# Kernel optimization log

Measured on AMD Instinct MI355X. Metric: run time of the kernel, lower is better.

The kernel has to match this reference:

```python
import jax, jax.numpy as jnp
import numpy as np

B, L, D_MODEL = 4, 2048, 1024
D_STATE, D_CONV, EXPAND, HEADDIM = 128, 4, 2, 64
D_INNER = EXPAND * D_MODEL            # 2048
NHEADS = D_INNER // HEADDIM           # 32
CONV_DIM = D_INNER + 2 * D_STATE      # 2304
D_IN_PROJ = 2 * D_INNER + 2 * D_STATE + NHEADS  # 4448
EPS = 1e-5


def _silu(v):
    return v * jax.nn.sigmoid(v)


def setup_inputs() -> dict:
    key = jax.random.key(0)
    ks = jax.random.split(key, 8)
    x = jax.random.normal(ks[0], (B, L, D_MODEL), dtype=jnp.float32)
    ln_w = jnp.ones((D_MODEL,), jnp.float32)
    ln_b = jnp.zeros((D_MODEL,), jnp.float32)
    in_proj_w = jax.random.normal(ks[1], (D_IN_PROJ, D_MODEL), jnp.float32) * 0.02
    conv_w = jax.random.normal(ks[2], (CONV_DIM, D_CONV), jnp.float32) * 0.2
    conv_b = jnp.zeros((CONV_DIM,), jnp.float32)
    # inverse-softplus of dt sampled in [1e-3, 1e-1], matching mamba2 dt init
    dt_bias = jnp.log(jnp.expm1(jax.random.uniform(ks[3], (NHEADS,), minval=0.001, maxval=0.1)))
    # A sampled uniform in [1,16], stored as log (A = -exp(A_log))
    A_log = jnp.log(jax.random.uniform(ks[4], (NHEADS,), minval=1.0, maxval=16.0))
    D = jnp.ones((NHEADS,), jnp.float32)
    rms_w = jnp.ones((D_INNER,), jnp.float32)
    out_proj_w = jax.random.normal(ks[5], (D_MODEL, D_INNER), jnp.float32) * 0.02
    return {"x": x, "ln_w": ln_w, "ln_b": ln_b, "in_proj_w": in_proj_w,
            "conv_w": conv_w, "conv_b": conv_b, "dt_bias": dt_bias,
            "A_log": A_log, "D": D, "rms_w": rms_w, "out_proj_w": out_proj_w}


def reference(x, ln_w, ln_b, in_proj_w, conv_w, conv_b, dt_bias, A_log, D, rms_w, out_proj_w):
    b = x.shape[0]
    # LayerNorm
    mu = x.mean(-1, keepdims=True)
    var = ((x - mu) ** 2).mean(-1, keepdims=True)
    u = (x - mu) * jax.lax.rsqrt(var + EPS) * ln_w + ln_b
    # input projection -> z | xBC | dt
    zxbcdt = jnp.einsum('bld,ed->ble', u, in_proj_w)
    z = zxbcdt[..., :D_INNER]
    xBC = zxbcdt[..., D_INNER:D_INNER + CONV_DIM]
    dt = jax.nn.softplus(zxbcdt[..., -NHEADS:] + dt_bias)  # (b,l,h)
    # causal depthwise conv along time (kernel D_CONV) + silu
    xpad = jnp.pad(xBC, ((0, 0), (D_CONV - 1, 0), (0, 0)))
    conv = conv_b + sum(conv_w[:, k] * xpad[:, k:k + L, :] for k in range(D_CONV))
    xBC = _silu(conv)
    xh = xBC[..., :D_INNER].reshape(b, L, NHEADS, HEADDIM)       # (b,l,h,p)
    Bm = xBC[..., D_INNER:D_INNER + D_STATE]                      # (b,l,n)
    Cm = xBC[..., D_INNER + D_STATE:]                             # (b,l,n)
    A = -jnp.exp(A_log)                                           # (h,)
    dA = jnp.exp(dt * A)                                          # (b,l,h)
    dtx = dt[..., None] * xh                                      # (b,l,h,p)

    def step(h, inp):
        dA_t, dtx_t, B_t, C_t = inp
        h = dA_t[:, :, None, None] * h + dtx_t[..., None] * B_t[:, None, None, :]
        y_t = jnp.einsum('bhpn,bn->bhp', h, C_t)
        return h, y_t

    h0 = jnp.zeros((b, NHEADS, HEADDIM, D_STATE), x.dtype)
    xs = (dA.transpose(1, 0, 2), dtx.transpose(1, 0, 2, 3),
          Bm.transpose(1, 0, 2), Cm.transpose(1, 0, 2))
    _, ys = jax.lax.scan(step, h0, xs)                            # (l,b,h,p)
    y = ys.transpose(1, 0, 2, 3) + D[None, None, :, None] * xh    # skip term
    y = y.reshape(b, L, D_INNER)
    # gated RMSNorm: rmsnorm(y * silu(z)) * weight
    g = y * _silu(z)
    g = g * jax.lax.rsqrt((g * g).mean(-1, keepdims=True) + EPS) * rms_w
    out = jnp.einsum('ble,de->bld', g, out_proj_w)
    # residual; dropout is identity in eval mode
    return out + x
```

## Files before the change

### kernel.cpp

```cpp
#include <hip/hip_runtime.h>
#include <hip/hip_bf16.h>

#define DEV __device__ __forceinline__

typedef unsigned short u16;
typedef unsigned int u32;
typedef float f32x4 __attribute__((ext_vector_type(4)));
typedef short s16x8 __attribute__((ext_vector_type(8)));

static constexpr int Bb = 4, Ll = 2048, DM = 1024, DI = 2048, NH = 32;
static constexpr int CD = 2304;
static constexpr int NP = 4384;
static constexpr int NP_PAD = 4480;
static constexpr int BL = Bb * Ll;
static constexpr int NC = 32;

DEV float u2f(u16 s) { return __uint_as_float(((u32)s) << 16); }
DEV u16 f2bu(float f) {
  __hip_bfloat16 h = __float2bfloat16(f);
  u16 s; __builtin_memcpy(&s, &h, 2); return s;
}
DEV float blo(u32 u) { return __uint_as_float(u << 16); }
DEV float bhi(u32 u) { return __uint_as_float(u & 0xffff0000u); }

DEV int swz64(int r, int k)  { return r * 64  + ((((k >> 3) ^ (r & 7))) << 3) + (k & 7); }

DEV void gl_lds16(const u16* g, u16* l) {
  __builtin_amdgcn_global_load_lds(
      (const __attribute__((address_space(1))) u32*)g,
      (__attribute__((address_space(3))) u32*)l, 16, 0, 0);
}

__global__ __launch_bounds__(256) void cvt_both(const float* __restrict__ w1,
    u16* __restrict__ W1b, const float* __restrict__ w2, u16* __restrict__ W2b) {
  const int total1 = NP_PAD * 1024;
  int i = blockIdx.x * 256 + threadIdx.x;
  if (i < total1) {
    int r = i >> 10;
    W1b[i] = (r < NP) ? f2bu(w1[i]) : (u16)0;
  } else {
    int j = i - total1;
    if (j < 1024 * 2048) W2b[j] = f2bu(w2[j]);
  }
}

__global__ __launch_bounds__(256) void ln_kernel(const float* __restrict__ x,
    const float* __restrict__ w, const float* __restrict__ bia, u16* __restrict__ u) {
  int row = blockIdx.x, tid = threadIdx.x;
  const float4* xr = (const float4*)(x + (size_t)row * DM);
  float4 v = xr[tid];
  float s = v.x + v.y + v.z + v.w;
  float s2 = v.x*v.x + v.y*v.y + v.z*v.z + v.w*v.w;
  #pragma unroll
  for (int o = 32; o; o >>= 1) { s += __shfl_down(s, o); s2 += __shfl_down(s2, o); }
  __shared__ float rs[4], rs2[4];
  int wv = tid >> 6, ln = tid & 63;
  if (ln == 0) { rs[wv] = s; rs2[wv] = s2; }
  __syncthreads();
  s = rs[0] + rs[1] + rs[2] + rs[3];
  s2 = rs2[0] + rs2[1] + rs2[2] + rs2[3];
  float mu = s * (1.f / DM);
  float var = s2 * (1.f / DM) - mu * mu;
  float inv = rsqrtf(var + 1e-5f);
  float4 wv4 = ((const float4*)w)[tid], bv4 = ((const float4*)bia)[tid];
  ushort4 o;
  o.x = f2bu((v.x - mu) * inv * wv4.x + bv4.x);
  o.y = f2bu((v.y - mu) * inv * wv4.y + bv4.y);
  o.z = f2bu((v.z - mu) * inv * wv4.z + bv4.z);
  o.w = f2bu((v.w - mu) * inv * wv4.w + bv4.w);
  ((ushort4*)(u + (size_t)row * DM))[tid] = o;
}

template<int MODE>
__global__ __launch_bounds__(512, 4) void gemm2p(const u16* __restrict__ A,
    const u16* __restrict__ Bw, void* __restrict__ o0, u16* __restrict__ xbc,
    u16* __restrict__ dtraw, const float* __restrict__ resid) {
  constexpr int K = (MODE == 0) ? 1024 : 2048;
  constexpr int NT = K / 32;
  __shared__ u16 SH[24576];
  int tid = threadIdx.x, wid = tid >> 6, lane = tid & 63;
  int fr = lane & 15, fq = lane >> 4;
  int nb = blockIdx.x;
  int xcd = nb & 7, i = nb >> 3;
  int m0 = (xcd * 4 + (i & 3)) * 256;
  int n0 = (i >> 2) * 128;
  int wm = (wid >> 1) * 64, wn = (wid & 1) * 64;
  int ksrcE = (((lane & 3) ^ ((lane >> 3) & 3)) << 3);
  int lr = lane >> 2;

  f32x4 acc[4][4];
  #pragma unroll
  for (int a = 0; a < 4; a++)
    #pragma unroll
    for (int b = 0; b < 4; b++) acc[a][b] = (f32x4){0.f, 0.f, 0.f, 0.f};

  auto STGA = [&](int t, int dstE) {
    #pragma unroll
    for (int h = 0; h < 2; h++) {
      int r0 = h * 128 + wid * 16;
      gl_lds16(A + (size_t)(m0 + r0 + lr) * K + t * 32 + ksrcE, &SH[dstE + r0 * 32]);
    }
  };
  auto STGB = [&](int t, int dstE) {
    int r0 = wid * 16;
    gl_lds16(Bw + (size_t)(n0 + r0 + lr) * K + t * 32 + ksrcE, &SH[dstE + r0 * 32]);
  };

  STGA(0, 0);
  STGB(0, 16384);
  asm volatile("s_waitcnt vmcnt(0)\n\ts_barrier" ::: "memory");
  for (int t = 0; t < NT; t++) {
    int ca = (t & 1) * 8192, cbf = 16384 + (t & 1) * 4096;
    if (t < NT - 1) {
      STGA(t + 1, ((t + 1) & 1) * 8192);
      STGB(t + 1, 16384 + ((t + 1) & 1) * 4096);
      asm volatile("s_waitcnt vmcnt(3)\n\ts_barrier" ::: "memory");
    } else {
      asm volatile("s_waitcnt vmcnt(0)\n\ts_barrier" ::: "memory");
    }
    s16x8 bB[4];
    #pragma unroll
    for (int nf = 0; nf < 4; nf++) {
      int rb = wn + nf * 16 + fr;
      bB[nf] = *(const s16x8*)&SH[cbf + rb * 32 + ((fq ^ ((rb >> 1) & 3)) << 3)];
    }
    __builtin_amdgcn_s_setprio(1);
    #pragma unroll
    for (int mf = 0; mf < 4; mf++) {
      int ra = wm + mf * 16 + fr;
      s16x8 af = *(const s16x8*)&SH[ca + ra * 32 + ((fq ^ ((ra >> 1) & 3)) << 3)];
      #pragma unroll
      for (int nf = 0; nf < 4; nf++)
        acc[mf][nf] = __builtin_amdgcn_mfma_f32_16x16x32_bf16(af, bB[nf], acc[mf][nf], 0, 0, 0);
    }
    __builtin_amdgcn_s_setprio(0);
    asm volatile("s_barrier" ::: "memory");
  }
  if (MODE == 0) {
    u16* zbuf = (u16*)o0;
    #pragma unroll
    for (int mf = 0; mf < 4; mf++) {
      #pragma unroll
      for (int nf = 0; nf < 4; nf++) {
        int col = n0 + wn + nf * 16 + fr;
        #pragma unroll
        for (int r = 0; r < 4; r++) {
          int row = m0 + wm + mf * 16 + fq * 4 + r;
          float v = acc[mf][nf][r];
          if (col < 2048)       zbuf[(size_t)row * 2048 + col] = f2bu(v);
          else if (col < 4352)  xbc[(size_t)row * 2304 + (col - 2048)] = f2bu(v);
          else if (col < 4384)  dtraw[(size_t)row * 32 + (col - 4352)] = f2bu(v);
        }
      }
    }
  } else {
    float* of = (float*)o0;
    #pragma unroll
    for (int mf = 0; mf < 4; mf++) {
      #pragma unroll
      for (int nf = 0; nf < 4; nf++) {
        int col = n0 + wn + nf * 16 + fr;
        #pragma unroll
        for (int r = 0; r < 4; r++) {
          int row = m0 + wm + mf * 16 + fq * 4 + r;
          of[(size_t)row * 1024 + col] = acc[mf][nf][r] + resid[(size_t)row * 1024 + col];
        }
      }
    }
  }
}

__global__ __launch_bounds__(256) void conv_silu(const u16* __restrict__ xbc,
    const float* __restrict__ cw, const float* __restrict__ cb, u16* __restrict__ out) {
  int i = blockIdx.x * 256 + threadIdx.x;
  if (i >= BL * (CD / 8)) return;
  int c8 = i % (CD / 8);
  int bl = i / (CD / 8);
  int l = bl & (Ll - 1);
  int c0 = c8 * 8;
  uint4 R[4];
  #pragma unroll
  for (int k = 0; k < 4; k++) {
    int ls = l - 3 + k;
    if (ls >= 0) R[k] = *(const uint4*)(xbc + (size_t)(bl - 3 + k) * CD + c0);
    else         R[k] = (uint4){0u, 0u, 0u, 0u};
  }
  u16 o[8];
  #pragma unroll
  for (int e = 0; e < 8; e++) {
    float acc = cb[c0 + e];
    float4 wv = *(const float4*)(cw + (size_t)(c0 + e) * 4);
    float wk[4] = {wv.x, wv.y, wv.z, wv.w};
    #pragma unroll
    for (int k = 0; k < 4; k++) {
      u32 word = (&R[k].x)[e >> 1];
      float xv = (e & 1) ? bhi(word) : blo(word);
      acc += wk[k] * xv;
    }
    float sg = 1.f / (1.f + __expf(-acc));
    o[e] = f2bu(acc * sg);
  }
  uint4 ov;
  ov.x = (u32)o[0] | ((u32)o[1] << 16);
  ov.y = (u32)o[2] | ((u32)o[3] << 16);
  ov.z = (u32)o[4] | ((u32)o[5] << 16);
  ov.w = (u32)o[6] | ((u32)o[7] << 16);
  *(uint4*)(out + (size_t)bl * CD + c0) = ov;
}

__global__ __launch_bounds__(256) void dt_cumsum(const u16* __restrict__ dtraw,
    const float* __restrict__ dtb, const float* __restrict__ alog,
    float* __restrict__ dtv, float* __restrict__ sv) {
  int wid = threadIdx.x >> 6, lane = threadIdx.x & 63;
  int g = blockIdx.x * 4 + wid;
  int b = g >> 10, h = (g >> 5) & 31, c = g & 31;
  int t = c * 64 + lane;
  float raw = u2f(dtraw[(size_t)(b * Ll + t) * 32 + h]);
  float v = raw + dtb[h];
  float dt = (v > 20.f) ? v : log1pf(__expf(v));
  float a = -dt * __expf(alog[h]);
  float s = a;
  #pragma unroll
  for (int o = 1; o < 64; o <<= 1) {
    float u = __shfl_up(s, o);
    if (lane >= o) s += u;
  }
  int idx = (b * 32 + h) * Ll + t;
  dtv[idx] = dt;
  sv[idx] = s;
}

__global__ __launch_bounds__(256) void chunk_state(const u16* __restrict__ conv,
    const float* __restrict__ dtv, const float* __restrict__ sv,
    u16* __restrict__ S) {
  __shared__ u16 xsT[64 * 64];
  __shared__ u16 BT[128 * 64];
  int gid = blockIdx.x;
  int h = gid & 31, c = (gid >> 5) & 31, b = gid >> 10;
  int bh = b * 32 + h;
  int tid = threadIdx.x, w = tid >> 6, lane = tid & 63;
  int fr = lane & 15, fq = lane >> 4;
  int j = tid & 63, pg = tid >> 6;
  int tb = c * 64;
  const float* svb = sv + (size_t)bh * Ll + tb;
  const float* dvb = dtv + (size_t)bh * Ll + tb;
  const u16* cvb = conv + (size_t)(b * Ll + tb) * CD;
  float s_last = svb[63];
  float wj = __expf(s_last - svb[j]) * dvb[j];
  const u16* rowp = cvb + (size_t)j * CD;
  #pragma unroll
  for (int rep = 0; rep < 2; rep++) {
    int p0 = rep * 32 + pg * 8;
    uint4 v = *(const uint4*)(rowp + h * 64 + p0);
    u32 va[4] = {v.x, v.y, v.z, v.w};
    #pragma unroll
    for (int e = 0; e < 4; e++) {
      xsT[swz64(p0 + 2 * e, j)]     = f2bu(blo(va[e]) * wj);
      xsT[swz64(p0 + 2 * e + 1, j)] = f2bu(bhi(va[e]) * wj);
    }
  }
  #pragma unroll
  for (int rep = 0; rep < 4; rep++) {
    int n0 = rep * 32 + pg * 8;
    uint4 v = *(const uint4*)(rowp + DI + n0);
    u32 va[4] = {v.x, v.y, v.z, v.w};
    #pragma unroll
    for (int e = 0; e < 4; e++) {
      BT[swz64(n0 + 2 * e, j)]     = (u16)(va[e] & 0xffffu);
      BT[swz64(n0 + 2 * e + 1, j)] = (u16)(va[e] >> 16);
    }
  }
  __syncthreads();
  f32x4 acc[4][2];
  #pragma unroll
  for (int mi = 0; mi < 4; mi++)
    #pragma unroll
    for (int ni = 0; ni < 2; ni++) acc[mi][ni] = (f32x4){0.f, 0.f, 0.f, 0.f};
  #pragma unroll
  for (int ks = 0; ks < 2; ks++) {
    int k8 = ks * 4 + fq;
    s16x8 bfv[2];
    #pragma unroll
    for (int ni = 0; ni < 2; ni++) {
      int rb = w * 32 + ni * 16 + fr;
      bfv[ni] = *(const s16x8*)&BT[rb * 64 + ((k8 ^ (rb & 7)) << 3)];
    }
    #pragma unroll
    for (int mi = 0; mi < 4; mi++) {
      int ra = mi * 16 + fr;
      s16x8 af = *(const s16x8*)&xsT[ra * 64 + ((k8 ^ (ra & 7)) << 3)];
      #pragma unroll
      for (int ni = 0; ni < 2; ni++)
        acc[mi][ni] = __builtin_amdgcn_mfma_f32_16x16x32_bf16(af, bfv[ni], acc[mi][ni], 0, 0, 0);
    }
  }
  u16* Sc = S + ((size_t)bh * NC + c) * 8192;
  #pragma unroll
  for (int mi = 0; mi < 4; mi++) {
    #pragma unroll
    for (int ni = 0; ni < 2; ni++) {
      int p = mi * 16 + fq * 4;
      int n = w * 32 + ni * 16 + fr;
      #pragma unroll
      for (int r = 0; r < 4; r++)
        Sc[(size_t)(p + r) * 128 + n] = f2bu(acc[mi][ni][r]);
    }
  }
}

__global__ __launch_bounds__(256) void state_pass(u16* __restrict__ S,
    const float* __restrict__ sv) {
  int bh = blockIdx.x >> 3, q = blockIdx.x & 7;
  int o = q * 1024 + threadIdx.x * 4;
  const float* svb = sv + (size_t)bh * Ll;
  u16* base = S + (size_t)bh * NC * 8192 + o;
  float acc[4] = {0.f, 0.f, 0.f, 0.f};
  for (int c = 0; c < NC; c++) {
    uint2 sc = *(const uint2*)(base + (size_t)c * 8192);
    uint2 pre;
    pre.x = (u32)f2bu(acc[0]) | ((u32)f2bu(acc[1]) << 16);
    pre.y = (u32)f2bu(acc[2]) | ((u32)f2bu(acc[3]) << 16);
    *(uint2*)(base + (size_t)c * 8192) = pre;
    float E = __expf(svb[c * 64 + 63]);
    acc[0] = E * acc[0] + blo(sc.x);
    acc[1] = E * acc[1] + bhi(sc.x);
    acc[2] = E * acc[2] + blo(sc.y);
    acc[3] = E * acc[3] + bhi(sc.y);
  }
}

__global__ __launch_bounds__(256) void chunk_out(const u16* __restrict__ conv,
    const u16* __restrict__ hstart, const float* __restrict__ dtv,
    const float* __restrict__ sv, const float* __restrict__ Dp,
    u16* __restrict__ yb) {
  __shared__ u16 Ct[64 * 128];
  __shared__ u16 Bt[64 * 128];
  __shared__ u16 Hs[64 * 128];
  __shared__ u16 xT[64 * 64];
  __shared__ u16 Ml[64 * 64];
  __shared__ float svl[64], dtl[64], pexl[64];
  int gid = blockIdx.x;
  int h = gid & 31, c = (gid >> 5) & 31, b = gid >> 10;
  int tid = threadIdx.x, w = tid >> 6, lane = tid & 63;
  int fr = lane & 15, fq = lane >> 4;
  int tb = c * 64;
  const u16* cvb = conv + ((size_t)b * Ll + tb) * CD;
  const u16* hsrc = hstart + (((size_t)(b * 32 + h)) * NC + c) * 8192;
  #pragma unroll
  for (int qq = 0; qq < 4; qq++) {
    int q = w * 4 + qq;
    int i = q * 4 + (lane >> 4);
    int s = lane & 15;
    int kc = ((s ^ (i & 7)) << 3);
    gl_lds16(cvb + (size_t)i * CD + 2176 + kc, &Ct[q * 512]);
    gl_lds16(cvb + (size_t)i * CD + 2048 + kc, &Bt[q * 512]);
    gl_lds16(hsrc + (size_t)i * 128 + kc, &Hs[q * 512]);
  }
  {
    int j = tid & 63, pg = tid >> 6;
    const u16* rowp = cvb + (size_t)j * CD + h * 64;
    #pragma unroll
    for (int rep = 0; rep < 2; rep++) {
      int p0 = rep * 32 + pg * 8;
      uint4 v = *(const uint4*)(rowp + p0);
      u32 va[4] = {v.x, v.y, v.z, v.w};
      #pragma unroll
      for (int e = 0; e < 4; e++) {
        xT[swz64(p0 + 2 * e, j)]     = (u16)(va[e] & 0xffffu);
        xT[swz64(p0 + 2 * e + 1, j)] = (u16)(va[e] >> 16);
      }
    }
  }
  if (tid < 64) {
    float s = sv[(size_t)(b * 32 + h) * Ll + tb + tid];
    svl[tid] = s;
    pexl[tid] = __expf(s);
    dtl[tid] = dtv[(size_t)(b * 32 + h) * Ll + tb + tid];
  }
  __syncthreads();
  f32x4 g2[4];
  #pragma unroll
  for (int mi = 0; mi < 4; mi++) g2[mi] = (f32x4){0.f, 0.f, 0.f, 0.f};
  int wj = w * 16;
  #pragma unroll
  for (int ks = 0; ks < 4; ks++) {
    int k8 = ks * 4 + fq;
    int rb = wj + fr;
    s16x8 bf = *(const s16x8*)&Bt[rb * 128 + ((k8 ^ (rb & 7)) << 3)];
    #pragma unroll
    for (int mi = 0; mi < 4; mi++) {
      int ra = mi * 16 + fr;
      s16x8 af = *(const s16x8*)&Ct[ra * 128 + ((k8 ^ (ra & 7)) << 3)];
      g2[mi] = __builtin_amdgcn_mfma_f32_16x16x32_bf16(af, bf, g2[mi], 0, 0, 0);
    }
  }
  #pragma unroll
  for (int mi = 0; mi < 4; mi++) {
    int jj = wj + fr;
    #pragma unroll
    for (int r = 0; r < 4; r++) {
      int ii = mi * 16 + fq * 4 + r;
      float v = 0.f;
      if (jj <= ii) v = g2[mi][r] * __expf(svl[ii] - svl[jj]) * dtl[jj];
      Ml[swz64(ii, jj)] = f2bu(v);
    }
  }
  __syncthreads();
  f32x4 aY[4], a4[4];
  #pragma unroll
  for (int mi = 0; mi < 4; mi++) { aY[mi] = (f32x4){0.f, 0.f, 0.f, 0.f}; a4[mi] = (f32x4){0.f, 0.f, 0.f, 0.f}; }
  int wp = w * 16;
  #pragma unroll
  for (int ks = 0; ks < 2; ks++) {
    int k8 = ks * 4 + fq;
    int rb = wp + fr;
    s16x8 bf = *(const s16x8*)&xT[rb * 64 + ((k8 ^ (rb & 7)) << 3)];
    #pragma unroll
    for (int mi = 0; mi < 4; mi++) {
      int ra = mi * 16 + fr;
      s16x8 af = *(const s16x8*)&Ml[ra * 64 + ((k8 ^ (ra & 7)) << 3)];
      aY[mi] = __builtin_amdgcn_mfma_f32_16x16x32_bf16(af, bf, aY[mi], 0, 0, 0);
    }
  }
  #pragma unroll
  for (int ks = 0; ks < 4; ks++) {
    int k8 = ks * 4 + fq;
    int rb = wp + fr;
    s16x8 bf = *(const s16x8*)&Hs[rb * 128 + ((k8 ^ (rb & 7)) << 3)];
    #pragma unroll
    for (int mi = 0; mi < 4; mi++) {
      int ra = mi * 16 + fr;
      s16x8 af = *(const s16x8*)&Ct[ra * 128 + ((k8 ^ (ra & 7)) << 3)];
      a4[mi] = __builtin_amdgcn_mfma_f32_16x16x32_bf16(af, bf, a4[mi], 0, 0, 0);
    }
  }
  float Dh = Dp[h];
  u16* yrow = yb + ((size_t)b * Ll + tb) * DI + h * 64;
  #pragma unroll
  for (int mi = 0; mi < 4; mi++) {
    int p = wp + fr;
    #pragma unroll
    for (int r = 0; r < 4; r++) {
      int i = mi * 16 + fq * 4 + r;
      float xh = u2f(xT[swz64(p, i)]);
      yrow[(size_t)i * DI + p] = f2bu(aY[mi][r] + pexl[i] * a4[mi][r] + Dh * xh);
    }
  }
}

__global__ __launch_bounds__(256) void gate_rms(const u16* __restrict__ y,
    const u16* __restrict__ zbuf, const float* __restrict__ rw, u16* __restrict__ g) {
  int bl = blockIdx.x, tid = threadIdx.x;
  uint4 yv = ((const uint4*)(y + (size_t)bl * DI))[tid];
  uint4 zv = ((const uint4*)(zbuf + (size_t)bl * DI))[tid];
  u32 ya[4] = {yv.x, yv.y, yv.z, yv.w};
  u32 za[4] = {zv.x, zv.y, zv.z, zv.w};
  float gv[8];
  float ss = 0.f;
  #pragma unroll
  for (int jx = 0; jx < 4; jx++) {
    float y0 = blo(ya[jx]), y1 = bhi(ya[jx]);
    float z0 = blo(za[jx]), z1 = bhi(za[jx]);
    float s0 = z0 / (1.f + __expf(-z0));
    float s1 = z1 / (1.f + __expf(-z1));
    gv[jx * 2] = y0 * s0; gv[jx * 2 + 1] = y1 * s1;
    ss += gv[jx * 2] * gv[jx * 2] + gv[jx * 2 + 1] * gv[jx * 2 + 1];
  }
  #pragma unroll
  for (int o = 32; o; o >>= 1) ss += __shfl_down(ss, o);
  __shared__ float red[4];
  int wv = tid >> 6, ln = tid & 63;
  if (ln == 0) red[wv] = ss;
  __syncthreads();
  ss = red[0] + red[1] + red[2] + red[3];
  float scale = rsqrtf(ss * (1.f / DI) + 1e-5f);
  const float* rwp = rw + tid * 8;
  ushort4 o0, o1;
  o0.x = f2bu(gv[0] * scale * rwp[0]); o0.y = f2bu(gv[1] * scale * rwp[1]);
  o0.z = f2bu(gv[2] * scale * rwp[2]); o0.w = f2bu(gv[3] * scale * rwp[3]);
  o1.x = f2bu(gv[4] * scale * rwp[4]); o1.y = f2bu(gv[5] * scale * rwp[5]);
  o1.z = f2bu(gv[6] * scale * rwp[6]); o1.w = f2bu(gv[7] * scale * rwp[7]);
  ushort4* gp = (ushort4*)(g + (size_t)bl * DI + tid * 8);
  gp[0] = o0; gp[1] = o1;
}

extern "C" void kernel_launch(void* const* d_in, const int* in_sizes, int n_in,
                              void* d_out, int out_size, void* d_ws, size_t ws_size,
                              hipStream_t stream) {
  const float* x    = (const float*)d_in[0];
  const float* lnw  = (const float*)d_in[1];
  const float* lnb  = (const float*)d_in[2];
  const float* w1   = (const float*)d_in[3];
  const float* cw   = (const float*)d_in[4];
  const float* cb   = (const float*)d_in[5];
  const float* dtb  = (const float*)d_in[6];
  const float* alog = (const float*)d_in[7];
  const float* Dp   = (const float*)d_in[8];
  const float* rw   = (const float*)d_in[9];
  const float* w2   = (const float*)d_in[10];

  char* ws = (char*)d_ws;
  u16*   ub     = (u16*)(ws + 0);
  u16*   W1b    = (u16*)(ws + 16777216);
  u16*   conv   = (u16*)(ws + 0);
  u16*   zbuf   = (u16*)(ws + 37748736);
  u16*   xbc    = (u16*)(ws + 71303168);
  u16*   dtraw  = (u16*)(ws + 109051904);
  u16*   Sbuf   = (u16*)(ws + 71303168);
  u16*   gb     = (u16*)(ws + 71303168);
  float* dtv    = (float*)(ws + 138412032);
  float* sv     = (float*)(ws + 139460608);
  u16*   yb     = (u16*)(ws + 140509184);
  u16*   W2b    = (u16*)(ws + 174063616);
  if (ws_size < 178257920u) return;

  float* out = (float*)d_out;

  int cvt_total = NP_PAD * 1024 + 1024 * 2048;
  cvt_both<<<(cvt_total + 255) / 256, 256, 0, stream>>>(w1, W1b, w2, W2b);
  ln_kernel<<<BL, 256, 0, stream>>>(x, lnw, lnb, ub);
  gemm2p<0><<<1120, 512, 0, stream>>>(ub, W1b, zbuf, xbc, dtraw, nullptr);
  conv_silu<<<(BL * (CD / 8)) / 256, 256, 0, stream>>>(xbc, cw, cb, conv);
  dt_cumsum<<<1024, 256, 0, stream>>>(dtraw, dtb, alog, dtv, sv);
  chunk_state<<<4096, 256, 0, stream>>>(conv, dtv, sv, Sbuf);
  state_pass<<<1024, 256, 0, stream>>>(Sbuf, sv);
  chunk_out<<<4096, 256, 0, stream>>>(conv, Sbuf, dtv, sv, Dp, yb);
  gate_rms<<<BL, 256, 0, stream>>>(yb, zbuf, rw, gb);
  gemm2p<1><<<256, 512, 0, stream>>>(gb, W2b, out, nullptr, nullptr, x);
}
```

Measured before the change: 325.6 us.

## Merge independent launches, widen state_pass vectors, trim chunk_out LDS usage

Merges layernorm with weight conversion, and conv+silu with the dt cumsum, into single horizontally fused launches, cutting two kernel launches and their tails. state_pass now handles 8 bf16 per thread with 128-bit accesses using half as many blocks. chunk_out loads the inter-chunk state straight into registers instead of staging it in LDS, and reuses the Bt buffer for the masked M matrix at the cost of an extra barrier. Together these reduce LDS footprint for higher occupancy and remove small-kernel overheads.

After: 314.6 us. 1.03x faster.

```diff
diff --git a/kernel.cpp b/kernel.cpp
--- a/kernel.cpp
+++ b/kernel.cpp
@@ -31,44 +31,46 @@
       (__attribute__((address_space(3))) u32*)l, 16, 0, 0);
 }
 
-__global__ __launch_bounds__(256) void cvt_both(const float* __restrict__ w1,
-    u16* __restrict__ W1b, const float* __restrict__ w2, u16* __restrict__ W2b) {
-  const int total1 = NP_PAD * 1024;
-  int i = blockIdx.x * 256 + threadIdx.x;
-  if (i < total1) {
-    int r = i >> 10;
-    W1b[i] = (r < NP) ? f2bu(w1[i]) : (u16)0;
+__global__ __launch_bounds__(256) void prep_kernel(const float* __restrict__ x,
+    const float* __restrict__ w, const float* __restrict__ bia, u16* __restrict__ u,
+    const float* __restrict__ w1, u16* __restrict__ W1b,
+    const float* __restrict__ w2, u16* __restrict__ W2b) {
+  __shared__ float rs[4], rs2[4];
+  int tid = threadIdx.x;
+  if (blockIdx.x < BL) {
+    int row = blockIdx.x;
+    const float4* xr = (const float4*)(x + (size_t)row * DM);
+    float4 v = xr[tid];
+    float s = v.x + v.y + v.z + v.w;
+    float s2 = v.x*v.x + v.y*v.y + v.z*v.z + v.w*v.w;
+    #pragma unroll
+    for (int o = 32; o; o >>= 1) { s += __shfl_down(s, o); s2 += __shfl_down(s2, o); }
+    int wv = tid >> 6, ln = tid & 63;
+    if (ln == 0) { rs[wv] = s; rs2[wv] = s2; }
+    __syncthreads();
+    s = rs[0] + rs[1] + rs[2] + rs[3];
+    s2 = rs2[0] + rs2[1] + rs2[2] + rs2[3];
+    float mu = s * (1.f / DM);
+    float var = s2 * (1.f / DM) - mu * mu;
+    float inv = rsqrtf(var + 1e-5f);
+    float4 wv4 = ((const float4*)w)[tid], bv4 = ((const float4*)bia)[tid];
+    ushort4 o;
+    o.x = f2bu((v.x - mu) * inv * wv4.x + bv4.x);
+    o.y = f2bu((v.y - mu) * inv * wv4.y + bv4.y);
+    o.z = f2bu((v.z - mu) * inv * wv4.z + bv4.z);
+    o.w = f2bu((v.w - mu) * inv * wv4.w + bv4.w);
+    ((ushort4*)(u + (size_t)row * DM))[tid] = o;
   } else {
-    int j = i - total1;
-    if (j < 1024 * 2048) W2b[j] = f2bu(w2[j]);
-  }
-}
-
-__global__ __launch_bounds__(256) void ln_kernel(const float* __restrict__ x,
-    const float* __restrict__ w, const float* __restrict__ bia, u16* __restrict__ u) {
-  int row = blockIdx.x, tid = threadIdx.x;
-  const float4* xr = (const float4*)(x + (size_t)row * DM);
-  float4 v = xr[tid];
-  float s = v.x + v.y + v.z + v.w;
-  float s2 = v.x*v.x + v.y*v.y + v.z*v.z + v.w*v.w;
-  #pragma unroll
-  for (int o = 32; o; o >>= 1) { s += __shfl_down(s, o); s2 += __shfl_down(s2, o); }
-  __shared__ float rs[4], rs2[4];
-  int wv = tid >> 6, ln = tid & 63;
-  if (ln == 0) { rs[wv] = s; rs2[wv] = s2; }
-  __syncthreads();
-  s = rs[0] + rs[1] + rs[2] + rs[3];
-  s2 = rs2[0] + rs2[1] + rs2[2] + rs2[3];
-  float mu = s * (1.f / DM);
-  float var = s2 * (1.f / DM) - mu * mu;
-  float inv = rsqrtf(var + 1e-5f);
-  float4 wv4 = ((const float4*)w)[tid], bv4 = ((const float4*)bia)[tid];
-  ushort4 o;
-  o.x = f2bu((v.x - mu) * inv * wv4.x + bv4.x);
-  o.y = f2bu((v.y - mu) * inv * wv4.y + bv4.y);
-  o.z = f2bu((v.z - mu) * inv * wv4.z + bv4.z);
-  o.w = f2bu((v.w - mu) * inv * wv4.w + bv4.w);
-  ((ushort4*)(u + (size_t)row * DM))[tid] = o;
+    const int total1 = NP_PAD * 1024;
+    int i = (blockIdx.x - BL) * 256 + tid;
+    if (i < total1) {
+      int r = i >> 10;
+      W1b[i] = (r < NP) ? f2bu(w1[i]) : (u16)0;
+    } else {
+      int j = i - total1;
+      if (j < 1024 * 2048) W2b[j] = f2bu(w2[j]);
+    }
+  }
 }
 
 template<int MODE>
@@ -170,64 +172,64 @@
   }
 }
 
-__global__ __launch_bounds__(256) void conv_silu(const u16* __restrict__ xbc,
-    const float* __restrict__ cw, const float* __restrict__ cb, u16* __restrict__ out) {
-  int i = blockIdx.x * 256 + threadIdx.x;
-  if (i >= BL * (CD / 8)) return;
-  int c8 = i % (CD / 8);
-  int bl = i / (CD / 8);
-  int l = bl & (Ll - 1);
-  int c0 = c8 * 8;
-  uint4 R[4];
-  #pragma unroll
-  for (int k = 0; k < 4; k++) {
-    int ls = l - 3 + k;
-    if (ls >= 0) R[k] = *(const uint4*)(xbc + (size_t)(bl - 3 + k) * CD + c0);
-    else         R[k] = (uint4){0u, 0u, 0u, 0u};
-  }
-  u16 o[8];
-  #pragma unroll
-  for (int e = 0; e < 8; e++) {
-    float acc = cb[c0 + e];
-    float4 wv = *(const float4*)(cw + (size_t)(c0 + e) * 4);
-    float wk[4] = {wv.x, wv.y, wv.z, wv.w};
+__global__ __launch_bounds__(256) void convdt_kernel(const u16* __restrict__ xbc,
+    const float* __restrict__ cw, const float* __restrict__ cb, u16* __restrict__ out,
+    const u16* __restrict__ dtraw, const float* __restrict__ dtb,
+    const float* __restrict__ alog, float* __restrict__ dtv, float* __restrict__ sv) {
+  const int CONV_BLOCKS = (BL * (CD / 8)) / 256;
+  if (blockIdx.x < CONV_BLOCKS) {
+    int i = blockIdx.x * 256 + threadIdx.x;
+    int c8 = i % (CD / 8);
+    int bl = i / (CD / 8);
+    int l = bl & (Ll - 1);
+    int c0 = c8 * 8;
+    uint4 R[4];
     #pragma unroll
     for (int k = 0; k < 4; k++) {
-      u32 word = (&R[k].x)[e >> 1];
-      float xv = (e & 1) ? bhi(word) : blo(word);
-      acc += wk[k] * xv;
-    }
-    float sg = 1.f / (1.f + __expf(-acc));
-    o[e] = f2bu(acc * sg);
-  }
-  uint4 ov;
-  ov.x = (u32)o[0] | ((u32)o[1] << 16);
-  ov.y = (u32)o[2] | ((u32)o[3] << 16);
-  ov.z = (u32)o[4] | ((u32)o[5] << 16);
-  ov.w = (u32)o[6] | ((u32)o[7] << 16);
-  *(uint4*)(out + (size_t)bl * CD + c0) = ov;
-}
-
-__global__ __launch_bounds__(256) void dt_cumsum(const u16* __restrict__ dtraw,
-    const float* __restrict__ dtb, const float* __restrict__ alog,
-    float* __restrict__ dtv, float* __restrict__ sv) {
-  int wid = threadIdx.x >> 6, lane = threadIdx.x & 63;
-  int g = blockIdx.x * 4 + wid;
-  int b = g >> 10, h = (g >> 5) & 31, c = g & 31;
-  int t = c * 64 + lane;
-  float raw = u2f(dtraw[(size_t)(b * Ll + t) * 32 + h]);
-  float v = raw + dtb[h];
-  float dt = (v > 20.f) ? v : log1pf(__expf(v));
-  float a = -dt * __expf(alog[h]);
-  float s = a;
-  #pragma unroll
-  for (int o = 1; o < 64; o <<= 1) {
-    float u = __shfl_up(s, o);
-    if (lane >= o) s += u;
-  }
-  int idx = (b * 32 + h) * Ll + t;
-  dtv[idx] = dt;
-  sv[idx] = s;
+      int ls = l - 3 + k;
+      if (ls >= 0) R[k] = *(const uint4*)(xbc + (size_t)(bl - 3 + k) * CD + c0);
+      else         R[k] = (uint4){0u, 0u, 0u, 0u};
+    }
+    u16 o[8];
+    #pragma unroll
+    for (int e = 0; e < 8; e++) {
+      float acc = cb[c0 + e];
+      float4 wv = *(const float4*)(cw + (size_t)(c0 + e) * 4);
+      float wk[4] = {wv.x, wv.y, wv.z, wv.w};
+      #pragma unroll
+      for (int k = 0; k < 4; k++) {
+        u32 word = (&R[k].x)[e >> 1];
+        float xv = (e & 1) ? bhi(word) : blo(word);
+        acc += wk[k] * xv;
+      }
+      float sg = 1.f / (1.f + __expf(-acc));
+      o[e] = f2bu(acc * sg);
+    }
+    uint4 ov;
+    ov.x = (u32)o[0] | ((u32)o[1] << 16);
+    ov.y = (u32)o[2] | ((u32)o[3] << 16);
+    ov.z = (u32)o[4] | ((u32)o[5] << 16);
+    ov.w = (u32)o[6] | ((u32)o[7] << 16);
+    *(uint4*)(out + (size_t)bl * CD + c0) = ov;
+  } else {
+    int wid = threadIdx.x >> 6, lane = threadIdx.x & 63;
+    int g = (blockIdx.x - CONV_BLOCKS) * 4 + wid;
+    int b = g >> 10, h = (g >> 5) & 31, c = g & 31;
+    int t = c * 64 + lane;
+    float raw = u2f(dtraw[(size_t)(b * Ll + t) * 32 + h]);
+    float v = raw + dtb[h];
+    float dt = (v > 20.f) ? v : log1pf(__expf(v));
+    float a = -dt * __expf(alog[h]);
+    float s = a;
+    #pragma unroll
+    for (int o = 1; o < 64; o <<= 1) {
+      float u = __shfl_up(s, o);
+      if (lane >= o) s += u;
+    }
+    int idx = (b * 32 + h) * Ll + t;
+    dtv[idx] = dt;
+    sv[idx] = s;
+  }
 }
 
 __global__ __launch_bounds__(256) void chunk_state(const u16* __restrict__ conv,
@@ -310,22 +312,26 @@
 
 __global__ __launch_bounds__(256) void state_pass(u16* __restrict__ S,
     const float* __restrict__ sv) {
-  int bh = blockIdx.x >> 3, q = blockIdx.x & 7;
-  int o = q * 1024 + threadIdx.x * 4;
+  int bh = blockIdx.x >> 2, q = blockIdx.x & 3;
+  int o = q * 2048 + threadIdx.x * 8;
   const float* svb = sv + (size_t)bh * Ll;
   u16* base = S + (size_t)bh * NC * 8192 + o;
-  float acc[4] = {0.f, 0.f, 0.f, 0.f};
+  float acc[8] = {0.f, 0.f, 0.f, 0.f, 0.f, 0.f, 0.f, 0.f};
   for (int c = 0; c < NC; c++) {
-    uint2 sc = *(const uint2*)(base + (size_t)c * 8192);
-    uint2 pre;
+    uint4 sc = *(const uint4*)(base + (size_t)c * 8192);
+    uint4 pre;
     pre.x = (u32)f2bu(acc[0]) | ((u32)f2bu(acc[1]) << 16);
     pre.y = (u32)f2bu(acc[2]) | ((u32)f2bu(acc[3]) << 16);
-    *(uint2*)(base + (size_t)c * 8192) = pre;
+    pre.z = (u32)f2bu(acc[4]) | ((u32)f2bu(acc[5]) << 16);
+    pre.w = (u32)f2bu(acc[6]) | ((u32)f2bu(acc[7]) << 16);
+    *(uint4*)(base + (size_t)c * 8192) = pre;
     float E = __expf(svb[c * 64 + 63]);
-    acc[0] = E * acc[0] + blo(sc.x);
-    acc[1] = E * acc[1] + bhi(sc.x);
-    acc[2] = E * acc[2] + blo(sc.y);
-    acc[3] = E * acc[3] + bhi(sc.y);
+    u32 wv[4] = {sc.x, sc.y, sc.z, sc.w};
+    #pragma unroll
+    for (int e = 0; e < 4; e++) {
+      acc[2 * e]     = E * acc[2 * e]     + blo(wv[e]);
+      acc[2 * e + 1] = E * acc[2 * e + 1] + bhi(wv[e]);
+    }
   }
 }
 
@@ -335,9 +341,7 @@
     u16* __restrict__ yb) {
   __shared__ u16 Ct[64 * 128];
   __shared__ u16 Bt[64 * 128];
-  __shared__ u16 Hs[64 * 128];
   __shared__ u16 xT[64 * 64];
-  __shared__ u16 Ml[64 * 64];
   __shared__ float svl[64], dtl[64], pexl[64];
   int gid = blockIdx.x;
   int h = gid & 31, c = (gid >> 5) & 31, b = gid >> 10;
@@ -346,6 +350,14 @@
   int tb = c * 64;
   const u16* cvb = conv + ((size_t)b * Ll + tb) * CD;
   const u16* hsrc = hstart + (((size_t)(b * 32 + h)) * NC + c) * 8192;
+  int wp = w * 16, wj = w * 16;
+  s16x8 h4[4];
+  #pragma unroll
+  for (int ks = 0; ks < 4; ks++) {
+    int rb = wp + fr;
+    int k8 = ks * 4 + fq;
+    h4[ks] = *(const s16x8*)(hsrc + (size_t)rb * 128 + k8 * 8);
+  }
   #pragma unroll
   for (int qq = 0; qq < 4; qq++) {
     int q = w * 4 + qq;
@@ -354,7 +366,6 @@
     int kc = ((s ^ (i & 7)) << 3);
     gl_lds16(cvb + (size_t)i * CD + 2176 + kc, &Ct[q * 512]);
     gl_lds16(cvb + (size_t)i * CD + 2048 + kc, &Bt[q * 512]);
-    gl_lds16(hsrc + (size_t)i * 128 + kc, &Hs[q * 512]);
   }
   {
     int j = tid & 63, pg = tid >> 6;
@@ -381,7 +392,6 @@
   f32x4 g2[4];
   #pragma unroll
   for (int mi = 0; mi < 4; mi++) g2[mi] = (f32x4){0.f, 0.f, 0.f, 0.f};
-  int wj = w * 16;
   #pragma unroll
   for (int ks = 0; ks < 4; ks++) {
     int k8 = ks * 4 + fq;
@@ -394,6 +404,7 @@
       g2[mi] = __builtin_amdgcn_mfma_f32_16x16x32_bf16(af, bf, g2[mi], 0, 0, 0);
     }
   }
+  u16 mv[4][4];
   #pragma unroll
   for (int mi = 0; mi < 4; mi++) {
     int jj = wj + fr;
@@ -402,14 +413,23 @@
       int ii = mi * 16 + fq * 4 + r;
       float v = 0.f;
       if (jj <= ii) v = g2[mi][r] * __expf(svl[ii] - svl[jj]) * dtl[jj];
-      Ml[swz64(ii, jj)] = f2bu(v);
+      mv[mi][r] = f2bu(v);
+    }
+  }
+  __syncthreads();
+  #pragma unroll
+  for (int mi = 0; mi < 4; mi++) {
+    int jj = wj + fr;
+    #pragma unroll
+    for (int r = 0; r < 4; r++) {
+      int ii = mi * 16 + fq * 4 + r;
+      Bt[swz64(ii, jj)] = mv[mi][r];
     }
   }
   __syncthreads();
   f32x4 aY[4], a4[4];
   #pragma unroll
   for (int mi = 0; mi < 4; mi++) { aY[mi] = (f32x4){0.f, 0.f, 0.f, 0.f}; a4[mi] = (f32x4){0.f, 0.f, 0.f, 0.f}; }
-  int wp = w * 16;
   #pragma unroll
   for (int ks = 0; ks < 2; ks++) {
     int k8 = ks * 4 + fq;
@@ -418,20 +438,18 @@
     #pragma unroll
     for (int mi = 0; mi < 4; mi++) {
       int ra = mi * 16 + fr;
-      s16x8 af = *(const s16x8*)&Ml[ra * 64 + ((k8 ^ (ra & 7)) << 3)];
+      s16x8 af = *(const s16x8*)&Bt[ra * 64 + ((k8 ^ (ra & 7)) << 3)];
       aY[mi] = __builtin_amdgcn_mfma_f32_16x16x32_bf16(af, bf, aY[mi], 0, 0, 0);
     }
   }
   #pragma unroll
   for (int ks = 0; ks < 4; ks++) {
     int k8 = ks * 4 + fq;
-    int rb = wp + fr;
-    s16x8 bf = *(const s16x8*)&Hs[rb * 128 + ((k8 ^ (rb & 7)) << 3)];
     #pragma unroll
     for (int mi = 0; mi < 4; mi++) {
       int ra = mi * 16 + fr;
       s16x8 af = *(const s16x8*)&Ct[ra * 128 + ((k8 ^ (ra & 7)) << 3)];
-      a4[mi] = __builtin_amdgcn_mfma_f32_16x16x32_bf16(af, bf, a4[mi], 0, 0, 0);
+      a4[mi] = __builtin_amdgcn_mfma_f32_16x16x32_bf16(af, h4[ks], a4[mi], 0, 0, 0);
     }
   }
   float Dh = Dp[h];
@@ -516,14 +534,13 @@
 
   float* out = (float*)d_out;
 
-  int cvt_total = NP_PAD * 1024 + 1024 * 2048;
-  cvt_both<<<(cvt_total + 255) / 256, 256, 0, stream>>>(w1, W1b, w2, W2b);
-  ln_kernel<<<BL, 256, 0, stream>>>(x, lnw, lnb, ub);
+  int cvt_blocks = (NP_PAD * 1024 + 1024 * 2048) / 256;
+  prep_kernel<<<BL + cvt_blocks, 256, 0, stream>>>(x, lnw, lnb, ub, w1, W1b, w2, W2b);
   gemm2p<0><<<1120, 512, 0, stream>>>(ub, W1b, zbuf, xbc, dtraw, nullptr);
-  conv_silu<<<(BL * (CD / 8)) / 256, 256, 0, stream>>>(xbc, cw, cb, conv);
-  dt_cumsum<<<1024, 256, 0, stream>>>(dtraw, dtb, alog, dtv, sv);
+  convdt_kernel<<<(BL * (CD / 8)) / 256 + 1024, 256, 0, stream>>>(
+      xbc, cw, cb, conv, dtraw, dtb, alog, dtv, sv);
   chunk_state<<<4096, 256, 0, stream>>>(conv, dtv, sv, Sbuf);
-  state_pass<<<1024, 256, 0, stream>>>(Sbuf, sv);
+  state_pass<<<512, 256, 0, stream>>>(Sbuf, sv);
   chunk_out<<<4096, 256, 0, stream>>>(conv, Sbuf, dtv, sv, Dp, yb);
   gate_rms<<<BL, 256, 0, stream>>>(yb, zbuf, rw, gb);
   gemm2p<1><<<256, 512, 0, stream>>>(gb, W2b, out, nullptr, nullptr, x);
```
